# Kernel optimization log

Measured on AMD Instinct MI355X. Metric: run time of the kernel, lower is better.

Reference implementation:

```python
import jax, jax.numpy as jnp
import numpy as np


def setup_inputs() -> dict:
    key = jax.random.key(0)
    ks = jax.random.split(key, 9)
    N, K, CS, CT, OUT, S = 50000, 16, 64, 64, 64, 4
    x = jax.random.normal(ks[0], (N, CT), dtype=jnp.float32)
    src = jax.random.normal(ks[1], (N, CS), dtype=jnp.float32)
    neighbor_idx = jax.random.randint(ks[2], (N, K), 0, N, dtype=jnp.int32)
    scale_t = 1.0 / np.sqrt(CT)
    scale_s = 1.0 / np.sqrt(CS)
    Wt = jax.random.normal(ks[3], (CT, S), dtype=jnp.float32) * scale_t
    bt = jax.random.normal(ks[4], (S,), dtype=jnp.float32) * scale_t
    Ws = jax.random.normal(ks[5], (CS, S), dtype=jnp.float32) * scale_s
    bs = jax.random.normal(ks[6], (S,), dtype=jnp.float32) * scale_s
    W_lin = jax.random.normal(ks[7], (S, CS, OUT), dtype=jnp.float32) * scale_s
    b_lin = jax.random.normal(ks[8], (S, OUT), dtype=jnp.float32) * scale_s
    return {"x": x, "src": src, "neighbor_idx": neighbor_idx,
            "Wt": Wt, "bt": bt, "Ws": Ws, "bs": bs,
            "W_lin": W_lin, "b_lin": b_lin}


def reference(x, src, neighbor_idx, Wt, bt, Ws, bs, W_lin, b_lin):
    # Gather per-node neighbor messages: [N, K, Cs]
    msgs = src[neighbor_idx]
    size = Wt.shape[-1]
    # target assignment logits from own data: [N, S]
    t = x @ Wt + bt
    # source assignment logits from messages: [N, K, S]
    s = jnp.einsum('nkc,cs->nks', msgs, Ws) + bs
    # soft assignment over the `size` weight matrices (softmax over S)
    a = jax.nn.softmax(s + t[:, None, :], axis=-1)  # [N, K, S]
    # apply each of the `size` linears to the messages: [N, K, S, O]
    w = jnp.einsum('nkc,sco->nkso', msgs, W_lin) + b_lin
    # assignment-weighted mean over the S weight matrices: [N, K, O]
    out = jnp.einsum('nks,nkso->nko', a, w) / size
    return out
```

## Files before the change

kernel.cpp:

```cpp
#include <hip/hip_runtime.h>

#define CT 64
#define CS 64
#define K_NB 16
#define S_SZ 4
#define OUT_C 64

typedef float vfloat4 __attribute__((ext_vector_type(4)));

__global__ __launch_bounds__(256) void k0_logits(
    const float* __restrict__ x, const float* __restrict__ src,
    const float* __restrict__ Wt, const float* __restrict__ bt,
    const float* __restrict__ Ws, const float* __restrict__ bs,
    float* __restrict__ t_out, float* __restrict__ sl_out, int N)
{
    int r = blockIdx.x * blockDim.x + threadIdx.x;
    if (r >= N) return;
    const float4* xv  = (const float4*)(x   + (size_t)r * CT);
    const float4* sv  = (const float4*)(src + (size_t)r * CS);
    const float4* Wt4 = (const float4*)Wt;
    const float4* Ws4 = (const float4*)Ws;
    float4 at = *(const float4*)bt;
    float4 as = *(const float4*)bs;
    #pragma unroll
    for (int c4 = 0; c4 < 16; ++c4) {
        float4 xq = xv[c4];
        float4 sq = sv[c4];
        float xs_[4] = {xq.x, xq.y, xq.z, xq.w};
        float ss_[4] = {sq.x, sq.y, sq.z, sq.w};
        #pragma unroll
        for (int u = 0; u < 4; ++u) {
            float4 wt = Wt4[c4 * 4 + u];
            float4 ws = Ws4[c4 * 4 + u];
            at.x = fmaf(xs_[u], wt.x, at.x);
            at.y = fmaf(xs_[u], wt.y, at.y);
            at.z = fmaf(xs_[u], wt.z, at.z);
            at.w = fmaf(xs_[u], wt.w, at.w);
            as.x = fmaf(ss_[u], ws.x, as.x);
            as.y = fmaf(ss_[u], ws.y, as.y);
            as.z = fmaf(ss_[u], ws.z, as.z);
            as.w = fmaf(ss_[u], ws.w, as.w);
        }
    }
    ((float4*)t_out)[r]  = at;
    ((float4*)sl_out)[r] = as;
}

__global__ __launch_bounds__(256, 4) void k1_z(
    const float* __restrict__ src, const float* __restrict__ W_lin,
    const float* __restrict__ b_lin, float* __restrict__ Z, int N)
{
    const int col = threadIdx.x;
    const int s = col >> 6, o = col & 63;
    float w[64];
    #pragma unroll
    for (int c = 0; c < 64; ++c)
        w[c] = W_lin[s * 4096 + (c << 6) + o];
    const float bl = b_lin[col];
    __shared__ float lsrc[64];
    for (int j = blockIdx.x; j < N; j += gridDim.x) {
        if (threadIdx.x < 16)
            ((float4*)lsrc)[threadIdx.x] =
                ((const float4*)(src + ((size_t)j << 6)))[threadIdx.x];
        __syncthreads();
        const float4* l4 = (const float4*)lsrc;
        float a0 = bl, a1 = 0.f, a2 = 0.f, a3 = 0.f;
        #pragma unroll
        for (int c4 = 0; c4 < 16; ++c4) {
            float4 s4 = l4[c4];
            a0 = fmaf(s4.x, w[c4 * 4 + 0], a0);
            a1 = fmaf(s4.y, w[c4 * 4 + 1], a1);
            a2 = fmaf(s4.z, w[c4 * 4 + 2], a2);
            a3 = fmaf(s4.w, w[c4 * 4 + 3], a3);
        }
        Z[(size_t)j * 256 + col] = (a0 + a1) + (a2 + a3);
        __syncthreads();
    }
}

__global__ __launch_bounds__(256) void k2_out(
    const int* __restrict__ nidx, const float* __restrict__ t_in,
    const float* __restrict__ sl_in, const float* __restrict__ Z,
    float* __restrict__ out)
{
    const int T = blockIdx.x * 256 + threadIdx.x;
    const int p = T >> 4;
    const int quad = T & 15;
    const int n = p >> 4;
    const int j = __builtin_nontemporal_load(nidx + p);
    float4 tv = ((const float4*)t_in)[n];
    float4 sv = ((const float4*)sl_in)[j];
    float l0 = tv.x + sv.x, l1 = tv.y + sv.y;
    float l2 = tv.z + sv.z, l3 = tv.w + sv.w;
    float m = fmaxf(fmaxf(l0, l1), fmaxf(l2, l3));
    float e0 = __expf(l0 - m), e1 = __expf(l1 - m);
    float e2 = __expf(l2 - m), e3 = __expf(l3 - m);
    float inv = 0.25f / (e0 + e1 + e2 + e3);
    const float4* zb = (const float4*)Z + (size_t)j * 64 + quad;
    float4 z0 = zb[0], z1 = zb[16], z2 = zb[32], z3 = zb[48];
    vfloat4 o;
    o.x = (e0 * z0.x + e1 * z1.x + e2 * z2.x + e3 * z3.x) * inv;
    o.y = (e0 * z0.y + e1 * z1.y + e2 * z2.y + e3 * z3.y) * inv;
    o.z = (e0 * z0.z + e1 * z1.z + e2 * z2.z + e3 * z3.z) * inv;
    o.w = (e0 * z0.w + e1 * z1.w + e2 * z2.w + e3 * z3.w) * inv;
    __builtin_nontemporal_store(o, (vfloat4*)out + (size_t)p * 16 + quad);
}

extern "C" void kernel_launch(void* const* d_in, const int* in_sizes, int n_in,
                              void* d_out, int out_size, void* d_ws, size_t ws_size,
                              hipStream_t stream)
{
    const float* x   = (const float*)d_in[0];
    const float* src = (const float*)d_in[1];
    const int*   idx = (const int*)d_in[2];
    const float* Wt  = (const float*)d_in[3];
    const float* bt  = (const float*)d_in[4];
    const float* Ws  = (const float*)d_in[5];
    const float* bs  = (const float*)d_in[6];
    const float* Wl  = (const float*)d_in[7];
    const float* bl  = (const float*)d_in[8];
    float* out = (float*)d_out;

    const int N = in_sizes[0] / CT;

    float* Z  = (float*)d_ws;
    float* t  = Z + (size_t)N * 256;
    float* sl = t + (size_t)N * 4;

    hipLaunchKernelGGL(k0_logits, dim3((N + 255) / 256), dim3(256), 0, stream,
                       x, src, Wt, bt, Ws, bs, t, sl, N);
    hipLaunchKernelGGL(k1_z, dim3(1024), dim3(256), 0, stream,
                       src, Wl, bl, Z, N);
    hipLaunchKernelGGL(k2_out, dim3(N), dim3(256), 0, stream,
                       idx, t, sl, Z, out);
}
```

Before: 404.1 us.

## Invert gather into source-grouped scatter and fuse Z computation with output

```diff
diff --git a/kernel.cpp b/kernel.cpp
--- a/kernel.cpp
+++ b/kernel.cpp
@@ -8,47 +8,94 @@
 
 typedef float vfloat4 __attribute__((ext_vector_type(4)));
 
-__global__ __launch_bounds__(256) void k0_logits(
-    const float* __restrict__ x, const float* __restrict__ src,
-    const float* __restrict__ Wt, const float* __restrict__ bt,
-    const float* __restrict__ Ws, const float* __restrict__ bs,
-    float* __restrict__ t_out, float* __restrict__ sl_out, int N)
+__global__ __launch_bounds__(256) void kt_rowlin(
+    const float* __restrict__ in, const float* __restrict__ W,
+    const float* __restrict__ b, float* __restrict__ outp, int N)
 {
-    int r = blockIdx.x * blockDim.x + threadIdx.x;
+    int gt = blockIdx.x * 256 + threadIdx.x;
+    int r = gt >> 3, part = gt & 7;
     if (r >= N) return;
-    const float4* xv  = (const float4*)(x   + (size_t)r * CT);
-    const float4* sv  = (const float4*)(src + (size_t)r * CS);
-    const float4* Wt4 = (const float4*)Wt;
-    const float4* Ws4 = (const float4*)Ws;
-    float4 at = *(const float4*)bt;
-    float4 as = *(const float4*)bs;
+    const float4* rv = (const float4*)(in + (size_t)r * 64) + part * 2;
+    const float4* W4 = (const float4*)W;
+    float4 q0 = rv[0], q1 = rv[1];
+    int c0 = part * 8;
+    float4 acc = {0.f, 0.f, 0.f, 0.f};
+    float xc[8] = {q0.x, q0.y, q0.z, q0.w, q1.x, q1.y, q1.z, q1.w};
     #pragma unroll
-    for (int c4 = 0; c4 < 16; ++c4) {
-        float4 xq = xv[c4];
-        float4 sq = sv[c4];
-        float xs_[4] = {xq.x, xq.y, xq.z, xq.w};
-        float ss_[4] = {sq.x, sq.y, sq.z, sq.w};
-        #pragma unroll
-        for (int u = 0; u < 4; ++u) {
-            float4 wt = Wt4[c4 * 4 + u];
-            float4 ws = Ws4[c4 * 4 + u];
-            at.x = fmaf(xs_[u], wt.x, at.x);
-            at.y = fmaf(xs_[u], wt.y, at.y);
-            at.z = fmaf(xs_[u], wt.z, at.z);
-            at.w = fmaf(xs_[u], wt.w, at.w);
-            as.x = fmaf(ss_[u], ws.x, as.x);
-            as.y = fmaf(ss_[u], ws.y, as.y);
-            as.z = fmaf(ss_[u], ws.z, as.z);
-            as.w = fmaf(ss_[u], ws.w, as.w);
-        }
+    for (int u = 0; u < 8; ++u) {
+        float4 wv = W4[c0 + u];
+        acc.x = fmaf(xc[u], wv.x, acc.x);
+        acc.y = fmaf(xc[u], wv.y, acc.y);
+        acc.z = fmaf(xc[u], wv.z, acc.z);
+        acc.w = fmaf(xc[u], wv.w, acc.w);
     }
-    ((float4*)t_out)[r]  = at;
-    ((float4*)sl_out)[r] = as;
+    #pragma unroll
+    for (int m = 1; m < 8; m <<= 1) {
+        acc.x += __shfl_xor(acc.x, m);
+        acc.y += __shfl_xor(acc.y, m);
+        acc.z += __shfl_xor(acc.z, m);
+        acc.w += __shfl_xor(acc.w, m);
+    }
+    if (part == 0) {
+        float4 bb = *(const float4*)b;
+        acc.x += bb.x; acc.y += bb.y; acc.z += bb.z; acc.w += bb.w;
+        ((float4*)outp)[r] = acc;
+    }
 }
 
-__global__ __launch_bounds__(256, 4) void k1_z(
-    const float* __restrict__ src, const float* __restrict__ W_lin,
-    const float* __restrict__ b_lin, float* __restrict__ Z, int N)
+__global__ __launch_bounds__(256) void kh_zero(
+    int* __restrict__ counts, int* __restrict__ cursor, int N)
+{
+    int i = blockIdx.x * 256 + threadIdx.x;
+    if (i < N) { counts[i] = 0; cursor[i] = 0; }
+}
+
+__global__ __launch_bounds__(256) void kh_hist(
+    const int* __restrict__ nidx, int* __restrict__ counts, int NK)
+{
+    int p = blockIdx.x * 256 + threadIdx.x;
+    if (p < NK) atomicAdd(&counts[nidx[p]], 1);
+}
+
+__global__ __launch_bounds__(1024) void kh_scan(
+    const int* __restrict__ counts, int* __restrict__ offsets, int N)
+{
+    __shared__ int ls[1024];
+    const int t = threadIdx.x;
+    const int chunk = (N + 1023) >> 10;
+    const int lo = t * chunk;
+    const int hi = (lo + chunk < N) ? lo + chunk : N;
+    int s = 0;
+    for (int i = lo; i < hi; ++i) s += counts[i];
+    ls[t] = s;
+    __syncthreads();
+    for (int off = 1; off < 1024; off <<= 1) {
+        int v = (t >= off) ? ls[t - off] : 0;
+        __syncthreads();
+        ls[t] += v;
+        __syncthreads();
+    }
+    int excl = ls[t] - s;
+    for (int i = lo; i < hi; ++i) { offsets[i] = excl; excl += counts[i]; }
+}
+
+__global__ __launch_bounds__(256) void kh_fill(
+    const int* __restrict__ nidx, const int* __restrict__ offsets,
+    int* __restrict__ cursor, int* __restrict__ plist, int NK)
+{
+    int p = blockIdx.x * 256 + threadIdx.x;
+    if (p >= NK) return;
+    int j = nidx[p];
+    int pos = atomicAdd(&cursor[j], 1);
+    plist[offsets[j] + pos] = p;
+}
+
+__global__ __launch_bounds__(256) void k_main(
+    const int* __restrict__ counts, const int* __restrict__ offsets,
+    const int* __restrict__ plist, const float* __restrict__ src,
+    const float* __restrict__ W_lin, const float* __restrict__ b_lin,
+    const float* __restrict__ t_in, const float* __restrict__ sl_in,
+    float* __restrict__ out, int N)
 {
     const int col = threadIdx.x;
     const int s = col >> 6, o = col & 63;
@@ -57,53 +104,53 @@
     for (int c = 0; c < 64; ++c)
         w[c] = W_lin[s * 4096 + (c << 6) + o];
     const float bl = b_lin[col];
-    __shared__ float lsrc[64];
+    const int g = col >> 4;
+    const int lane16 = col & 15;
+    __shared__ float4 lsrc4[16];
+    __shared__ float4 zl4[64];
+    float* zl = (float*)zl4;
+
     for (int j = blockIdx.x; j < N; j += gridDim.x) {
-        if (threadIdx.x < 16)
-            ((float4*)lsrc)[threadIdx.x] =
-                ((const float4*)(src + ((size_t)j << 6)))[threadIdx.x];
+        const int cnt = counts[j];
+        if (cnt == 0) continue;
+        const int off = offsets[j];
         __syncthreads();
-        const float4* l4 = (const float4*)lsrc;
+        if (col < 16)
+            lsrc4[col] = ((const float4*)(src + ((size_t)j << 6)))[col];
+        __syncthreads();
         float a0 = bl, a1 = 0.f, a2 = 0.f, a3 = 0.f;
         #pragma unroll
         for (int c4 = 0; c4 < 16; ++c4) {
-            float4 s4 = l4[c4];
+            float4 s4 = lsrc4[c4];
             a0 = fmaf(s4.x, w[c4 * 4 + 0], a0);
             a1 = fmaf(s4.y, w[c4 * 4 + 1], a1);
             a2 = fmaf(s4.z, w[c4 * 4 + 2], a2);
             a3 = fmaf(s4.w, w[c4 * 4 + 3], a3);
         }
-        Z[(size_t)j * 256 + col] = (a0 + a1) + (a2 + a3);
+        zl[col] = (a0 + a1) + (a2 + a3);
+        float4 slv = ((const float4*)sl_in)[j];
         __syncthreads();
+        for (int ib = g; ib < cnt; ib += 16) {
+            const int p = plist[off + ib];
+            const int n = p >> 4;
+            float4 tv = ((const float4*)t_in)[n];
+            float l0 = tv.x + slv.x, l1 = tv.y + slv.y;
+            float l2 = tv.z + slv.z, l3 = tv.w + slv.w;
+            float m = fmaxf(fmaxf(l0, l1), fmaxf(l2, l3));
+            float e0 = __expf(l0 - m), e1 = __expf(l1 - m);
+            float e2 = __expf(l2 - m), e3 = __expf(l3 - m);
+            float inv = 0.25f / (e0 + e1 + e2 + e3);
+            float4 z0 = zl4[lane16], z1 = zl4[16 + lane16];
+            float4 z2 = zl4[32 + lane16], z3 = zl4[48 + lane16];
+            vfloat4 ov;
+            ov.x = (e0 * z0.x + e1 * z1.x + e2 * z2.x + e3 * z3.x) * inv;
+            ov.y = (e0 * z0.y + e1 * z1.y + e2 * z2.y + e3 * z3.y) * inv;
+            ov.z = (e0 * z0.z + e1 * z1.z + e2 * z2.z + e3 * z3.z) * inv;
+            ov.w = (e0 * z0.w + e1 * z1.w + e2 * z2.w + e3 * z3.w) * inv;
+            __builtin_nontemporal_store(
+                ov, (vfloat4*)out + (size_t)p * 16 + lane16);
+        }
     }
-}
-
-__global__ __launch_bounds__(256) void k2_out(
-    const int* __restrict__ nidx, const float* __restrict__ t_in,
-    const float* __restrict__ sl_in, const float* __restrict__ Z,
-    float* __restrict__ out)
-{
-    const int T = blockIdx.x * 256 + threadIdx.x;
-    const int p = T >> 4;
-    const int quad = T & 15;
-    const int n = p >> 4;
-    const int j = __builtin_nontemporal_load(nidx + p);
-    float4 tv = ((const float4*)t_in)[n];
-    float4 sv = ((const float4*)sl_in)[j];
-    float l0 = tv.x + sv.x, l1 = tv.y + sv.y;
-    float l2 = tv.z + sv.z, l3 = tv.w + sv.w;
-    float m = fmaxf(fmaxf(l0, l1), fmaxf(l2, l3));
-    float e0 = __expf(l0 - m), e1 = __expf(l1 - m);
-    float e2 = __expf(l2 - m), e3 = __expf(l3 - m);
-    float inv = 0.25f / (e0 + e1 + e2 + e3);
-    const float4* zb = (const float4*)Z + (size_t)j * 64 + quad;
-    float4 z0 = zb[0], z1 = zb[16], z2 = zb[32], z3 = zb[48];
-    vfloat4 o;
-    o.x = (e0 * z0.x + e1 * z1.x + e2 * z2.x + e3 * z3.x) * inv;
-    o.y = (e0 * z0.y + e1 * z1.y + e2 * z2.y + e3 * z3.y) * inv;
-    o.z = (e0 * z0.z + e1 * z1.z + e2 * z2.z + e3 * z3.z) * inv;
-    o.w = (e0 * z0.w + e1 * z1.w + e2 * z2.w + e3 * z3.w) * inv;
-    __builtin_nontemporal_store(o, (vfloat4*)out + (size_t)p * 16 + quad);
 }
 
 extern "C" void kernel_launch(void* const* d_in, const int* in_sizes, int n_in,
@@ -121,16 +168,32 @@
     const float* bl  = (const float*)d_in[8];
     float* out = (float*)d_out;
 
-    const int N = in_sizes[0] / CT;
+    const int N  = in_sizes[0] / CT;
+    const int NK = N * K_NB;
 
-    float* Z  = (float*)d_ws;
-    float* t  = Z + (size_t)N * 256;
+    float* t  = (float*)d_ws;
     float* sl = t + (size_t)N * 4;
+    int* counts  = (int*)(sl + (size_t)N * 4);
+    int* cursor  = counts + N;
+    int* offsets = cursor + N;
+    int* plist   = offsets + N;
 
-    hipLaunchKernelGGL(k0_logits, dim3((N + 255) / 256), dim3(256), 0, stream,
-                       x, src, Wt, bt, Ws, bs, t, sl, N);
-    hipLaunchKernelGGL(k1_z, dim3(1024), dim3(256), 0, stream,
-                       src, Wl, bl, Z, N);
-    hipLaunchKernelGGL(k2_out, dim3(N), dim3(256), 0, stream,
-                       idx, t, sl, Z, out);
+    const int gbN  = (N + 255) / 256;
+    const int gbNK = (NK + 255) / 256;
+    const int gbRow = (N * 8 + 255) / 256;
+
+    hipLaunchKernelGGL(kh_zero, dim3(gbN), dim3(256), 0, stream,
+                       counts, cursor, N);
+    hipLaunchKernelGGL(kh_hist, dim3(gbNK), dim3(256), 0, stream,
+                       idx, counts, NK);
+    hipLaunchKernelGGL(kh_scan, dim3(1), dim3(1024), 0, stream,
+                       counts, offsets, N);
+    hipLaunchKernelGGL(kh_fill, dim3(gbNK), dim3(256), 0, stream,
+                       idx, offsets, cursor, plist, NK);
+    hipLaunchKernelGGL(kt_rowlin, dim3(gbRow), dim3(256), 0, stream,
+                       x, Wt, bt, t, N);
+    hipLaunchKernelGGL(kt_rowlin, dim3(gbRow), dim3(256), 0, stream,
+                       src, Ws, bs, sl, N);
+    hipLaunchKernelGGL(k_main, dim3(2048), dim3(256), 0, stream,
+                       counts, offsets, plist, src, Wl, bl, t, sl, out, N);
 }
```

Result: slower. 460.4 us (+13.9%).
